# Performance work log

Hardware: AMD Instinct MI355X
Metric: run time of the kernel (lower is better)

The kernel has to match this reference:

```python
import math
import jax, jax.numpy as jnp
import numpy as np

B, N, C = 2, 2048, 768
H, DH = 12, 64  # num_heads, head_dim


def setup_inputs() -> dict:
    key = jax.random.key(0)
    ks = jax.random.split(key, 5)
    s = 1.0 / math.sqrt(C)  # keep linear outputs O(1)
    return {
        "x": jax.random.normal(ks[0], (B, N, C), jnp.float32),
        "Wq": jax.random.normal(ks[1], (C, C), jnp.float32) * s,
        "bq": jnp.zeros((C,), jnp.float32),
        "Wk": jax.random.normal(ks[2], (C, C), jnp.float32) * s,
        "bk": jnp.zeros((C,), jnp.float32),
        "Wv": jax.random.normal(ks[3], (C, C), jnp.float32) * s,
        "bv": jnp.zeros((C,), jnp.float32),
        "Wp": jax.random.normal(ks[4], (C, C), jnp.float32) * s,
        "bp": jnp.zeros((C,), jnp.float32),
    }


def reference(x, Wq, bq, Wk, bk, Wv, bv, Wp, bp):
    # Linear projections; torch nn.Linear computes x @ W.T + b, here W stored
    # as (in, out) so it's x @ W + b with equivalent math.
    def split(t):  # [B,N,C] -> [B,H,N,DH]
        return t.reshape(B, N, H, DH).transpose(0, 2, 1, 3)

    q = split(x @ Wq + bq)
    k = split(x @ Wk + bk)
    v = split(x @ Wv + bv)
    scale = 1.0 / math.sqrt(DH)
    attn = jnp.einsum("bhqd,bhkd->bhqk", q, k) * scale  # [B,H,N,N]
    attn = jax.nn.softmax(attn, axis=-1)  # attn_drop=0.0 -> identity
    y = jnp.einsum("bhqk,bhkd->bhqd", attn, v)  # [B,H,N,DH]
    y = y.transpose(0, 2, 1, 3).reshape(B, N, C)
    return y @ Wp + bp  # proj_drop=0.0 -> identity
```

## Files before the change

### kernel.cpp

```cpp
#include <hip/hip_runtime.h>


typedef __bf16 bf16_t;
typedef __bf16 bf16x8 __attribute__((ext_vector_type(8)));
typedef __bf16 bf16x4 __attribute__((ext_vector_type(4)));
typedef short  short4_t __attribute__((ext_vector_type(4)));
typedef float  floatx4 __attribute__((ext_vector_type(4)));

#define MFMA32(a, b, c) __builtin_amdgcn_mfma_f32_16x16x32_bf16(a, b, c, 0, 0, 0)
#define MFMA16(a, b, c) __builtin_amdgcn_mfma_f32_16x16x16bf16_1k(a, b, c, 0, 0, 0)

__global__ __launch_bounds__(256) void cvt_x_kernel(const float* __restrict__ x,
                                                    bf16_t* __restrict__ xb) {
  int i = blockIdx.x * 256 + threadIdx.x;
  floatx4 v = ((const floatx4*)x)[i];
  bf16x4 o;
  o[0] = (bf16_t)v[0]; o[1] = (bf16_t)v[1]; o[2] = (bf16_t)v[2]; o[3] = (bf16_t)v[3];
  ((bf16x4*)xb)[i] = o;
}

__global__ __launch_bounds__(256) void cvt_wt_kernel(
    const float* __restrict__ W0, const float* __restrict__ W1,
    const float* __restrict__ W2, const float* __restrict__ W3,
    bf16_t* __restrict__ T0, bf16_t* __restrict__ T1,
    bf16_t* __restrict__ T2, bf16_t* __restrict__ T3) {
  const int z = blockIdx.z;
  const float* W = (z == 0) ? W0 : (z == 1) ? W1 : (z == 2) ? W2 : W3;
  bf16_t* WT = (z == 0) ? T0 : (z == 1) ? T1 : (z == 2) ? T2 : T3;
  __shared__ bf16_t T[64][65];
  const int c = threadIdx.x & 63, r0 = threadIdx.x >> 6;
  const int i0 = blockIdx.y * 64, o0 = blockIdx.x * 64;
#pragma unroll
  for (int p = 0; p < 16; ++p) {
    int r = p * 4 + r0;
    T[r][c] = (bf16_t)W[(i0 + r) * 768 + o0 + c];
  }
  __syncthreads();
#pragma unroll
  for (int p = 0; p < 16; ++p) {
    int r = p * 4 + r0;
    WT[(o0 + r) * 768 + i0 + c] = T[c][r];
  }
}

#define LDP 40

__global__ __launch_bounds__(256) void gemm_qkv(
    const bf16_t* __restrict__ Xb, const bf16_t* __restrict__ WqT,
    const bf16_t* __restrict__ WkT, const bf16_t* __restrict__ WvT,
    const float* __restrict__ bq, const float* __restrict__ bk,
    const float* __restrict__ bv, bf16_t* __restrict__ qw,
    bf16_t* __restrict__ kw, bf16_t* __restrict__ vtw) {
  __shared__ bf16_t Al[128 * LDP];
  __shared__ bf16_t Bl[128 * LDP];
  const int z = blockIdx.z;
  const bf16_t* Wt = (z == 0) ? WqT : (z == 1) ? WkT : WvT;
  const float* bias = (z == 0) ? bq : (z == 1) ? bk : bv;
  const float oscale = (z == 0) ? 0.18033688011112042f : 1.0f;

  const int tid = threadIdx.x, lane = tid & 63, w = tid >> 6;
  const int wr = w >> 1, wc = w & 1;
  const int l15 = lane & 15, quad = lane >> 4;
  const int m0 = blockIdx.y * 128, n0 = blockIdx.x * 128;

  floatx4 acc[4][4] = {};

  for (int kt = 0; kt < 768; kt += 32) {
#pragma unroll
    for (int p = 0; p < 2; ++p) {
      int c = p * 256 + tid;
      int row = c >> 2, qo = (c & 3) * 8;
      *(bf16x8*)&Al[row * LDP + qo] = *(const bf16x8*)&Wt[(m0 + row) * 768 + kt + qo];
      *(bf16x8*)&Bl[row * LDP + qo] = *(const bf16x8*)&Xb[(n0 + row) * 768 + kt + qo];
    }
    __syncthreads();
    bf16x8 af[4], bfr[4];
#pragma unroll
    for (int i = 0; i < 4; ++i) {
      af[i]  = *(bf16x8*)&Al[(wr * 64 + i * 16 + l15) * LDP + quad * 8];
      bfr[i] = *(bf16x8*)&Bl[(wc * 64 + i * 16 + l15) * LDP + quad * 8];
    }
#pragma unroll
    for (int mi = 0; mi < 4; ++mi)
#pragma unroll
      for (int ni = 0; ni < 4; ++ni)
        acc[mi][ni] = MFMA32(af[mi], bfr[ni], acc[mi][ni]);
    __syncthreads();
  }

  const int hh = (m0 + wr * 64) >> 6;
#pragma unroll
  for (int mi = 0; mi < 4; ++mi) {
    const int d0 = mi * 16 + quad * 4;
    const int gm0 = m0 + wr * 64 + d0;
    float bv4[4];
#pragma unroll
    for (int r = 0; r < 4; ++r) bv4[r] = bias[gm0 + r];
#pragma unroll
    for (int ni = 0; ni < 4; ++ni) {
      const int gn = n0 + wc * 64 + ni * 16 + l15;
      const int bb = gn >> 11, tok = gn & 2047;
      if (z < 2) {
        bf16_t* o = (z == 0) ? qw : kw;
        bf16x4 pk;
#pragma unroll
        for (int r = 0; r < 4; ++r)
          pk[r] = (bf16_t)((acc[mi][ni][r] + bv4[r]) * oscale);
        *(bf16x4*)&o[(((bb * 12 + hh) * 2048 + tok) << 6) + d0] = pk;
      } else {
#pragma unroll
        for (int r = 0; r < 4; ++r)
          vtw[(((bb * 12 + hh) << 6) + d0 + r) * 2048 + tok] =
              (bf16_t)(acc[mi][ni][r] + bv4[r]);
      }
    }
  }
}

__global__ __launch_bounds__(256) void gemm_proj(
    const bf16_t* __restrict__ Yb, const bf16_t* __restrict__ WpT,
    const float* __restrict__ bias, float* __restrict__ out) {
  __shared__ bf16_t Al[128 * LDP];
  __shared__ bf16_t Bl[128 * LDP];
  const int tid = threadIdx.x, lane = tid & 63, w = tid >> 6;
  const int wr = w >> 1, wc = w & 1;
  const int l15 = lane & 15, quad = lane >> 4;
  const int m0 = blockIdx.y * 128, n0 = blockIdx.x * 128;

  floatx4 acc[4][4] = {};

  for (int kt = 0; kt < 768; kt += 32) {
#pragma unroll
    for (int p = 0; p < 2; ++p) {
      int c = p * 256 + tid;
      int row = c >> 2, qo = (c & 3) * 8;
      *(bf16x8*)&Al[row * LDP + qo] = *(const bf16x8*)&WpT[(m0 + row) * 768 + kt + qo];
      *(bf16x8*)&Bl[row * LDP + qo] = *(const bf16x8*)&Yb[(n0 + row) * 768 + kt + qo];
    }
    __syncthreads();
    bf16x8 af[4], bfr[4];
#pragma unroll
    for (int i = 0; i < 4; ++i) {
      af[i]  = *(bf16x8*)&Al[(wr * 64 + i * 16 + l15) * LDP + quad * 8];
      bfr[i] = *(bf16x8*)&Bl[(wc * 64 + i * 16 + l15) * LDP + quad * 8];
    }
#pragma unroll
    for (int mi = 0; mi < 4; ++mi)
#pragma unroll
      for (int ni = 0; ni < 4; ++ni)
        acc[mi][ni] = MFMA32(af[mi], bfr[ni], acc[mi][ni]);
    __syncthreads();
  }

#pragma unroll
  for (int mi = 0; mi < 4; ++mi) {
    const int gm0 = m0 + wr * 64 + mi * 16 + quad * 4;
    floatx4 bv4;
#pragma unroll
    for (int r = 0; r < 4; ++r) bv4[r] = bias[gm0 + r];
#pragma unroll
    for (int ni = 0; ni < 4; ++ni) {
      const int gn = n0 + wc * 64 + ni * 16 + l15;
      floatx4 v = acc[mi][ni] + bv4;
      *(floatx4*)&out[gn * 768 + gm0] = v;
    }
  }
}

__global__ __launch_bounds__(256) void attn_kernel(
    const bf16_t* __restrict__ Q, const bf16_t* __restrict__ Kg,
    const bf16_t* __restrict__ Vt, bf16_t* __restrict__ Y) {
  constexpr int AKP = 72, AVP = 136;
  __shared__ bf16_t Kl[128 * AKP];
  __shared__ bf16_t Vl[64 * AVP];
  __shared__ float Sm[4][16];
  const int tid = threadIdx.x, lane = tid & 63, w = tid >> 6;
  const int l15 = lane & 15, quad = lane >> 4;
  const int bh = blockIdx.y;
  const int q0 = blockIdx.x * 64;
  const bf16_t* Qb = Q + bh * 2048 * 64;
  const bf16_t* Kb = Kg + bh * 2048 * 64;
  const bf16_t* Vb = Vt + bh * 64 * 2048;

  bf16x8 qf[2];
#pragma unroll
  for (int kk = 0; kk < 2; ++kk)
    qf[kk] = *(const bf16x8*)&Qb[(q0 + w * 16 + l15) * 64 + kk * 32 + quad * 8];

  floatx4 oacc[4] = {};
  float lsum = 0.f;

  for (int kt = 0; kt < 16; ++kt) {
    const int key0 = kt * 128;
#pragma unroll
    for (int p = 0; p < 4; ++p) {
      int c = p * 256 + tid;
      int kr = c >> 3, kq = (c & 7) * 8;
      *(bf16x8*)&Kl[kr * AKP + kq] = *(const bf16x8*)&Kb[(key0 + kr) * 64 + kq];
      int vr = c >> 4, vq = (c & 15) * 8;
      *(bf16x8*)&Vl[vr * AVP + vq] = *(const bf16x8*)&Vb[vr * 2048 + key0 + vq];
    }
    __syncthreads();

    floatx4 s[8] = {};
#pragma unroll
    for (int nk = 0; nk < 8; ++nk)
#pragma unroll
      for (int kk = 0; kk < 2; ++kk) {
        bf16x8 kf = *(bf16x8*)&Kl[(nk * 16 + l15) * AKP + kk * 32 + quad * 8];
        s[nk] = MFMA32(kf, qf[kk], s[nk]);
      }

    short4_t pk[8];
#pragma unroll
    for (int nk = 0; nk < 8; ++nk) {
      bf16x4 ph;
#pragma unroll
      for (int r = 0; r < 4; ++r) {
        const float pv = __builtin_amdgcn_exp2f(s[nk][r]);
        lsum += pv;
        ph[r] = (bf16_t)pv;
      }
      pk[nk] = __builtin_bit_cast(short4_t, ph);
    }

#pragma unroll
    for (int nk = 0; nk < 8; ++nk)
#pragma unroll
      for (int nd = 0; nd < 4; ++nd) {
        bf16x4 vf = *(bf16x4*)&Vl[(nd * 16 + l15) * AVP + nk * 16 + quad * 4];
        oacc[nd] = MFMA16(pk[nk], __builtin_bit_cast(short4_t, vf), oacc[nd]);
      }
    __syncthreads();
  }

  lsum += __shfl_xor(lsum, 16);
  lsum += __shfl_xor(lsum, 32);
  Sm[w][l15] = lsum;
  __builtin_amdgcn_fence(__ATOMIC_SEQ_CST, "wavefront");
  const int bb = bh / 12, h = bh % 12;
#pragma unroll
  for (int r = 0; r < 4; ++r) {
    const float inv = 1.f / Sm[w][quad * 4 + r];
    const int tok = q0 + w * 16 + quad * 4 + r;
#pragma unroll
    for (int nd = 0; nd < 4; ++nd) {
      const int col = h * 64 + nd * 16 + l15;
      Y[(bb * 2048 + tok) * 768 + col] = (bf16_t)(oacc[nd][r] * inv);
    }
  }
}

extern "C" void kernel_launch(void* const* d_in, const int* in_sizes, int n_in,
                              void* d_out, int out_size, void* d_ws, size_t ws_size,
                              hipStream_t stream) {
  const float* x  = (const float*)d_in[0];
  const float* Wq = (const float*)d_in[1];
  const float* bq = (const float*)d_in[2];
  const float* Wk = (const float*)d_in[3];
  const float* bk = (const float*)d_in[4];
  const float* Wv = (const float*)d_in[5];
  const float* bv = (const float*)d_in[6];
  const float* Wp = (const float*)d_in[7];
  const float* bp = (const float*)d_in[8];
  float* out = (float*)d_out;

  char* ws = (char*)d_ws;
  bf16_t* xb  = (bf16_t*)ws; ws += (size_t)4096 * 768 * 2;
  bf16_t* WqT = (bf16_t*)ws; ws += (size_t)768 * 768 * 2;
  bf16_t* WkT = (bf16_t*)ws; ws += (size_t)768 * 768 * 2;
  bf16_t* WvT = (bf16_t*)ws; ws += (size_t)768 * 768 * 2;
  bf16_t* WpT = (bf16_t*)ws; ws += (size_t)768 * 768 * 2;
  bf16_t* qw  = (bf16_t*)ws; ws += (size_t)24 * 2048 * 64 * 2;
  bf16_t* kw  = (bf16_t*)ws; ws += (size_t)24 * 2048 * 64 * 2;
  bf16_t* vtw = (bf16_t*)ws; ws += (size_t)24 * 2048 * 64 * 2;
  bf16_t* yw  = (bf16_t*)ws; ws += (size_t)4096 * 768 * 2;

  cvt_x_kernel<<<3072, 256, 0, stream>>>(x, xb);
  cvt_wt_kernel<<<dim3(12, 12, 4), 256, 0, stream>>>(Wq, Wk, Wv, Wp, WqT, WkT, WvT, WpT);

  gemm_qkv<<<dim3(32, 6, 3), 256, 0, stream>>>(xb, WqT, WkT, WvT, bq, bk, bv, qw, kw, vtw);
  attn_kernel<<<dim3(32, 24), 256, 0, stream>>>(qw, kw, vtw, yw);
  gemm_proj<<<dim3(32, 6), 256, 0, stream>>>(yw, WpT, bp, out);
}
```

Measured before the change: 208.9 us.

## Split attention keys across waves and double GEMM K-tile depth

The attention kernel now gives each wave a 32-key slice of every 128-key tile across all 64 queries, instead of giving each wave 16 queries over all keys. Partial outputs and row sums are then reduced through shared memory in bf16 at the end. This reuses each K/V fragment read from LDS across four query tiles, cutting LDS traffic per MFMA, but it adds a cross-wave reduction and bf16 rounding of partial sums. Separately, both GEMMs move from a 32 to a 64 K-step per tile, halving the number of barriers and loop iterations at the cost of more LDS.

```diff
diff --git a/kernel.cpp b/kernel.cpp
--- a/kernel.cpp
+++ b/kernel.cpp
@@ -43,7 +43,7 @@
   }
 }
 
-#define LDP 40
+#define LDPG 72
 
 __global__ __launch_bounds__(256) void gemm_qkv(
     const bf16_t* __restrict__ Xb, const bf16_t* __restrict__ WqT,
@@ -51,8 +51,8 @@
     const float* __restrict__ bq, const float* __restrict__ bk,
     const float* __restrict__ bv, bf16_t* __restrict__ qw,
     bf16_t* __restrict__ kw, bf16_t* __restrict__ vtw) {
-  __shared__ bf16_t Al[128 * LDP];
-  __shared__ bf16_t Bl[128 * LDP];
+  __shared__ bf16_t Al[128 * LDPG];
+  __shared__ bf16_t Bl[128 * LDPG];
   const int z = blockIdx.z;
   const bf16_t* Wt = (z == 0) ? WqT : (z == 1) ? WkT : WvT;
   const float* bias = (z == 0) ? bq : (z == 1) ? bk : bv;
@@ -65,26 +65,29 @@
 
   floatx4 acc[4][4] = {};
 
-  for (int kt = 0; kt < 768; kt += 32) {
-#pragma unroll
-    for (int p = 0; p < 2; ++p) {
+  for (int kt = 0; kt < 768; kt += 64) {
+#pragma unroll
+    for (int p = 0; p < 4; ++p) {
       int c = p * 256 + tid;
-      int row = c >> 2, qo = (c & 3) * 8;
-      *(bf16x8*)&Al[row * LDP + qo] = *(const bf16x8*)&Wt[(m0 + row) * 768 + kt + qo];
-      *(bf16x8*)&Bl[row * LDP + qo] = *(const bf16x8*)&Xb[(n0 + row) * 768 + kt + qo];
-    }
-    __syncthreads();
-    bf16x8 af[4], bfr[4];
-#pragma unroll
-    for (int i = 0; i < 4; ++i) {
-      af[i]  = *(bf16x8*)&Al[(wr * 64 + i * 16 + l15) * LDP + quad * 8];
-      bfr[i] = *(bf16x8*)&Bl[(wc * 64 + i * 16 + l15) * LDP + quad * 8];
-    }
-#pragma unroll
-    for (int mi = 0; mi < 4; ++mi)
-#pragma unroll
-      for (int ni = 0; ni < 4; ++ni)
-        acc[mi][ni] = MFMA32(af[mi], bfr[ni], acc[mi][ni]);
+      int row = c >> 3, qo = (c & 7) * 8;
+      *(bf16x8*)&Al[row * LDPG + qo] = *(const bf16x8*)&Wt[(m0 + row) * 768 + kt + qo];
+      *(bf16x8*)&Bl[row * LDPG + qo] = *(const bf16x8*)&Xb[(n0 + row) * 768 + kt + qo];
+    }
+    __syncthreads();
+#pragma unroll
+    for (int kk = 0; kk < 2; ++kk) {
+      bf16x8 af[4], bfr[4];
+#pragma unroll
+      for (int i = 0; i < 4; ++i) {
+        af[i]  = *(bf16x8*)&Al[(wr * 64 + i * 16 + l15) * LDPG + kk * 32 + quad * 8];
+        bfr[i] = *(bf16x8*)&Bl[(wc * 64 + i * 16 + l15) * LDPG + kk * 32 + quad * 8];
+      }
+#pragma unroll
+      for (int mi = 0; mi < 4; ++mi)
+#pragma unroll
+        for (int ni = 0; ni < 4; ++ni)
+          acc[mi][ni] = MFMA32(af[mi], bfr[ni], acc[mi][ni]);
+    }
     __syncthreads();
   }
 
@@ -120,8 +123,8 @@
 __global__ __launch_bounds__(256) void gemm_proj(
     const bf16_t* __restrict__ Yb, const bf16_t* __restrict__ WpT,
     const float* __restrict__ bias, float* __restrict__ out) {
-  __shared__ bf16_t Al[128 * LDP];
-  __shared__ bf16_t Bl[128 * LDP];
+  __shared__ bf16_t Al[128 * LDPG];
+  __shared__ bf16_t Bl[128 * LDPG];
   const int tid = threadIdx.x, lane = tid & 63, w = tid >> 6;
   const int wr = w >> 1, wc = w & 1;
   const int l15 = lane & 15, quad = lane >> 4;
@@ -129,26 +132,29 @@
 
   floatx4 acc[4][4] = {};
 
-  for (int kt = 0; kt < 768; kt += 32) {
-#pragma unroll
-    for (int p = 0; p < 2; ++p) {
+  for (int kt = 0; kt < 768; kt += 64) {
+#pragma unroll
+    for (int p = 0; p < 4; ++p) {
       int c = p * 256 + tid;
-      int row = c >> 2, qo = (c & 3) * 8;
-      *(bf16x8*)&Al[row * LDP + qo] = *(const bf16x8*)&WpT[(m0 + row) * 768 + kt + qo];
-      *(bf16x8*)&Bl[row * LDP + qo] = *(const bf16x8*)&Yb[(n0 + row) * 768 + kt + qo];
-    }
-    __syncthreads();
-    bf16x8 af[4], bfr[4];
-#pragma unroll
-    for (int i = 0; i < 4; ++i) {
-      af[i]  = *(bf16x8*)&Al[(wr * 64 + i * 16 + l15) * LDP + quad * 8];
-      bfr[i] = *(bf16x8*)&Bl[(wc * 64 + i * 16 + l15) * LDP + quad * 8];
-    }
-#pragma unroll
-    for (int mi = 0; mi < 4; ++mi)
-#pragma unroll
-      for (int ni = 0; ni < 4; ++ni)
-        acc[mi][ni] = MFMA32(af[mi], bfr[ni], acc[mi][ni]);
+      int row = c >> 3, qo = (c & 7) * 8;
+      *(bf16x8*)&Al[row * LDPG + qo] = *(const bf16x8*)&WpT[(m0 + row) * 768 + kt + qo];
+      *(bf16x8*)&Bl[row * LDPG + qo] = *(const bf16x8*)&Yb[(n0 + row) * 768 + kt + qo];
+    }
+    __syncthreads();
+#pragma unroll
+    for (int kk = 0; kk < 2; ++kk) {
+      bf16x8 af[4], bfr[4];
+#pragma unroll
+      for (int i = 0; i < 4; ++i) {
+        af[i]  = *(bf16x8*)&Al[(wr * 64 + i * 16 + l15) * LDPG + kk * 32 + quad * 8];
+        bfr[i] = *(bf16x8*)&Bl[(wc * 64 + i * 16 + l15) * LDPG + kk * 32 + quad * 8];
+      }
+#pragma unroll
+      for (int mi = 0; mi < 4; ++mi)
+#pragma unroll
+        for (int ni = 0; ni < 4; ++ni)
+          acc[mi][ni] = MFMA32(af[mi], bfr[ni], acc[mi][ni]);
+    }
     __syncthreads();
   }
 
@@ -171,9 +177,12 @@
     const bf16_t* __restrict__ Q, const bf16_t* __restrict__ Kg,
     const bf16_t* __restrict__ Vt, bf16_t* __restrict__ Y) {
   constexpr int AKP = 72, AVP = 136;
-  __shared__ bf16_t Kl[128 * AKP];
-  __shared__ bf16_t Vl[64 * AVP];
-  __shared__ float Sm[4][16];
+  __shared__ __align__(16) char smem[128 * AKP * 2 + 64 * AVP * 2];
+  bf16_t* Kl = (bf16_t*)smem;
+  bf16_t* Vl = (bf16_t*)(smem + 128 * AKP * 2);
+  bf16_t* Ox = (bf16_t*)smem;
+  float*  Ls = (float*)(smem + 32768);
+
   const int tid = threadIdx.x, lane = tid & 63, w = tid >> 6;
   const int l15 = lane & 15, quad = lane >> 4;
   const int bh = blockIdx.y;
@@ -182,13 +191,15 @@
   const bf16_t* Kb = Kg + bh * 2048 * 64;
   const bf16_t* Vb = Vt + bh * 64 * 2048;
 
-  bf16x8 qf[2];
-#pragma unroll
-  for (int kk = 0; kk < 2; ++kk)
-    qf[kk] = *(const bf16x8*)&Qb[(q0 + w * 16 + l15) * 64 + kk * 32 + quad * 8];
-
-  floatx4 oacc[4] = {};
-  float lsum = 0.f;
+  bf16x8 qf[4][2];
+#pragma unroll
+  for (int ni = 0; ni < 4; ++ni)
+#pragma unroll
+    for (int kk = 0; kk < 2; ++kk)
+      qf[ni][kk] = *(const bf16x8*)&Qb[(q0 + ni * 16 + l15) * 64 + kk * 32 + quad * 8];
+
+  floatx4 oacc[4][4] = {};
+  float lsum[4] = {0.f, 0.f, 0.f, 0.f};
 
   for (int kt = 0; kt < 16; ++kt) {
     const int key0 = kt * 128;
@@ -202,51 +213,86 @@
     }
     __syncthreads();
 
-    floatx4 s[8] = {};
-#pragma unroll
-    for (int nk = 0; nk < 8; ++nk)
+    floatx4 s[2][4] = {};
+#pragma unroll
+    for (int mt = 0; mt < 2; ++mt)
 #pragma unroll
       for (int kk = 0; kk < 2; ++kk) {
-        bf16x8 kf = *(bf16x8*)&Kl[(nk * 16 + l15) * AKP + kk * 32 + quad * 8];
-        s[nk] = MFMA32(kf, qf[kk], s[nk]);
-      }
-
-    short4_t pk[8];
-#pragma unroll
-    for (int nk = 0; nk < 8; ++nk) {
-      bf16x4 ph;
-#pragma unroll
-      for (int r = 0; r < 4; ++r) {
-        const float pv = __builtin_amdgcn_exp2f(s[nk][r]);
-        lsum += pv;
-        ph[r] = (bf16_t)pv;
-      }
-      pk[nk] = __builtin_bit_cast(short4_t, ph);
-    }
-
-#pragma unroll
-    for (int nk = 0; nk < 8; ++nk)
+        bf16x8 kf = *(bf16x8*)&Kl[(w * 32 + mt * 16 + l15) * AKP + kk * 32 + quad * 8];
+#pragma unroll
+        for (int ni = 0; ni < 4; ++ni)
+          s[mt][ni] = MFMA32(kf, qf[ni][kk], s[mt][ni]);
+      }
+
+    short4_t pk[2][4];
+#pragma unroll
+    for (int mt = 0; mt < 2; ++mt)
+#pragma unroll
+      for (int ni = 0; ni < 4; ++ni) {
+        bf16x4 ph;
+#pragma unroll
+        for (int r = 0; r < 4; ++r) {
+          const float pv = __builtin_amdgcn_exp2f(s[mt][ni][r]);
+          lsum[ni] += pv;
+          ph[r] = (bf16_t)pv;
+        }
+        pk[mt][ni] = __builtin_bit_cast(short4_t, ph);
+      }
+
+#pragma unroll
+    for (int mt = 0; mt < 2; ++mt)
 #pragma unroll
       for (int nd = 0; nd < 4; ++nd) {
-        bf16x4 vf = *(bf16x4*)&Vl[(nd * 16 + l15) * AVP + nk * 16 + quad * 4];
-        oacc[nd] = MFMA16(pk[nk], __builtin_bit_cast(short4_t, vf), oacc[nd]);
-      }
-    __syncthreads();
-  }
-
-  lsum += __shfl_xor(lsum, 16);
-  lsum += __shfl_xor(lsum, 32);
-  Sm[w][l15] = lsum;
-  __builtin_amdgcn_fence(__ATOMIC_SEQ_CST, "wavefront");
+        bf16x4 vf = *(bf16x4*)&Vl[(nd * 16 + l15) * AVP + w * 32 + mt * 16 + quad * 4];
+        short4_t vs = __builtin_bit_cast(short4_t, vf);
+#pragma unroll
+        for (int ni = 0; ni < 4; ++ni)
+          oacc[ni][nd] = MFMA16(pk[mt][ni], vs, oacc[ni][nd]);
+      }
+    __syncthreads();
+  }
+
+#pragma unroll
+  for (int ni = 0; ni < 4; ++ni) {
+    lsum[ni] += __shfl_xor(lsum[ni], 16);
+    lsum[ni] += __shfl_xor(lsum[ni], 32);
+  }
+
+#pragma unroll
+  for (int ni = 0; ni < 4; ++ni)
+#pragma unroll
+    for (int nd = 0; nd < 4; ++nd) {
+      bf16x4 ob;
+#pragma unroll
+      for (int r = 0; r < 4; ++r) ob[r] = (bf16_t)oacc[ni][nd][r];
+      *(bf16x4*)&Ox[(((nd * 4 + w) * 4 + ni) * 64 + lane) * 4] = ob;
+    }
+  if (quad == 0) {
+#pragma unroll
+    for (int ni = 0; ni < 4; ++ni) Ls[(w * 4 + ni) * 16 + l15] = lsum[ni];
+  }
+  __syncthreads();
+
   const int bb = bh / 12, h = bh % 12;
-#pragma unroll
-  for (int r = 0; r < 4; ++r) {
-    const float inv = 1.f / Sm[w][quad * 4 + r];
-    const int tok = q0 + w * 16 + quad * 4 + r;
-#pragma unroll
-    for (int nd = 0; nd < 4; ++nd) {
-      const int col = h * 64 + nd * 16 + l15;
-      Y[(bb * 2048 + tok) * 768 + col] = (bf16_t)(oacc[nd][r] * inv);
+  const int col = h * 64 + w * 16 + l15;
+#pragma unroll
+  for (int ni = 0; ni < 4; ++ni) {
+    floatx4 ofin = oacc[ni][w];
+#pragma unroll
+    for (int src = 0; src < 4; ++src) {
+      if (src == w) continue;
+      bf16x4 ob = *(bf16x4*)&Ox[(((w * 4 + src) * 4 + ni) * 64 + lane) * 4];
+#pragma unroll
+      for (int r = 0; r < 4; ++r) ofin[r] += (float)ob[r];
+    }
+#pragma unroll
+    for (int r = 0; r < 4; ++r) {
+      const float tot = Ls[(0 * 4 + ni) * 16 + quad * 4 + r] +
+                        Ls[(1 * 4 + ni) * 16 + quad * 4 + r] +
+                        Ls[(2 * 4 + ni) * 16 + quad * 4 + r] +
+                        Ls[(3 * 4 + ni) * 16 + quad * 4 + r];
+      const int tok = q0 + ni * 16 + quad * 4 + r;
+      Y[(bb * 2048 + tok) * 768 + col] = (bf16_t)(ofin[r] / tot);
     }
   }
 }
```

Measured after the change: 401.1 us. 92.0% more time.
